# Kernel tuning notes

Hardware: AMD Instinct MI355X
Metric: run time of the kernel (lower is better)

The kernel has to match this reference:

```python
import jax, jax.numpy as jnp
import numpy as np

B = 65536

def setup_inputs() -> dict:
    key = jax.random.key(0)
    ks = jax.random.split(key, 8)
    x = jax.random.normal(ks[0], (B, 784), dtype=jnp.float32)
    conv_w = jnp.ones((3, 3), dtype=jnp.float32)  # Parameter(ones((3,3)))
    # Linear layers (stored as [in, out] so forward is x @ W + b)
    w1 = jax.random.normal(ks[1], (676, 100), dtype=jnp.float32) * 0.04
    b1 = jnp.zeros((100,), dtype=jnp.float32)
    w2 = jax.random.normal(ks[2], (100, 10), dtype=jnp.float32) * 0.1
    b2 = jnp.zeros((10,), dtype=jnp.float32)
    w3 = jax.random.normal(ks[3], (10, 10), dtype=jnp.float32) * 0.3
    b3 = jnp.zeros((10,), dtype=jnp.float32)
    return {"x": x, "conv_w": conv_w, "w1": w1, "b1": b1,
            "w2": w2, "b2": b2, "w3": w3, "b3": b3}


def _convolve_batch(x, conv_w):
    # x: [B, 28, 28]; valid 3x3 correlation (tensordot of patch with weight, no flip)
    lhs = x[:, None, :, :]                 # [B, 1, 28, 28] NCHW
    rhs = conv_w[None, None, :, :]         # [1, 1, 3, 3] OIHW
    out = jax.lax.conv_general_dilated(
        lhs, rhs, window_strides=(1, 1), padding="VALID",
        dimension_numbers=("NCHW", "OIHW", "NCHW"))
    return out[:, 0]                       # [B, 26, 26]


def reference(x, conv_w, w1, b1, w2, b2, w3, b3):
    b = x.shape[0]
    h = _convolve_batch(x.reshape(b, 28, 28), conv_w)   # [B, 26, 26]
    h = h.reshape(b, 676)
    h = jax.nn.relu(h @ w1 + b1)
    h = jax.nn.relu(h @ w2 + b2)
    return h @ w3 + b3                                   # [B, 10]
```

## Files before the change

kernel.cpp:

```cpp
#include <hip/hip_runtime.h>
#include <hip/hip_bf16.h>

#define K1 784
#define N1 100
#define KT 25
#define NTT 7
#define NTP 8

typedef __attribute__((ext_vector_type(8))) short bf16x8;
typedef __attribute__((ext_vector_type(4))) float f32x4;

__device__ __forceinline__ ushort f2bf(float f) {
    union { float f; unsigned u; } v; v.f = f;
    unsigned u = v.u;
    return (ushort)((u + 0x7FFFu + ((u >> 16) & 1u)) >> 16);
}

__device__ __forceinline__ bf16x8 pack_bf16x8(float4 a, float4 b) {
    union { unsigned u[4]; bf16x8 v; } r;
    asm("v_cvt_pk_bf16_f32 %0, %1, %2" : "=v"(r.u[0]) : "v"(a.x), "v"(a.y));
    asm("v_cvt_pk_bf16_f32 %0, %1, %2" : "=v"(r.u[1]) : "v"(a.z), "v"(a.w));
    asm("v_cvt_pk_bf16_f32 %0, %1, %2" : "=v"(r.u[2]) : "v"(b.x), "v"(b.y));
    asm("v_cvt_pk_bf16_f32 %0, %1, %2" : "=v"(r.u[3]) : "v"(b.z), "v"(b.w));
    return r.v;
}

__device__ __forceinline__ void gload_lds16(const void* g, void* l) {
    __builtin_amdgcn_global_load_lds(
        (const __attribute__((address_space(1))) void*)g,
        (__attribute__((address_space(3))) void*)l, 16, 0, 0);
}

__global__ void build_wp(const float* __restrict__ w1,
                         const float* __restrict__ conv_w,
                         ushort* __restrict__ wp) {
    int idx = blockIdx.x * blockDim.x + threadIdx.x;
    if (idx >= KT * NTP * 512) return;
    int j = idx & 7, lane = (idx >> 3) & 63, rest = idx >> 9;
    int nt = rest & 7, kt = rest >> 3;
    int k = kt * 32 + (lane >> 4) * 8 + j;
    int n = nt * 16 + (lane & 15);
    float w = 0.f;
    if (k < K1 && n < N1) {
        int py = k / 28, px = k % 28;
        #pragma unroll
        for (int dy = 0; dy < 3; ++dy) {
            int oy = py - dy; if (oy < 0 || oy > 25) continue;
            #pragma unroll
            for (int dx = 0; dx < 3; ++dx) {
                int ox = px - dx; if (ox < 0 || ox > 25) continue;
                w += conv_w[dy * 3 + dx] * w1[(oy * 26 + ox) * N1 + n];
            }
        }
    }
    wp[(size_t)(kt * NTP + nt) * 512 + lane * 8 + j] = f2bf(w);
}

__global__ __launch_bounds__(256, 2) void fused_mfma(
    const float* __restrict__ x, const ushort* __restrict__ wp,
    const float* __restrict__ b1, const float* __restrict__ w2,
    const float* __restrict__ b2, const float* __restrict__ w3,
    const float* __restrict__ b3, float* __restrict__ out)
{
    __shared__ __attribute__((aligned(16))) ushort bsm[3][NTP * 512];
    __shared__ float w2t[10][112];
    __shared__ float w3s[100];
    __shared__ float b1s[100];
    __shared__ float b2s[10], b3s[10];

    const int tid  = threadIdx.x;
    const int lane = tid & 63;
    const int lo16 = lane & 15, hi4 = lane >> 4;
    const int wid  = tid >> 6;
    const size_t rowbase = (size_t)blockIdx.x * 128 + wid * 32;

    for (int e = tid; e < 10 * 112; e += 256) w2t[e / 112][e % 112] = 0.f;
    __syncthreads();
    for (int e = tid; e < 1000; e += 256) w2t[e % 10][e / 10] = w2[e];
    for (int e = tid; e < 100; e += 256) { w3s[e] = w3[e]; b1s[e] = b1[e]; }
    if (tid < 10) { b2s[tid] = b2[tid]; b3s[tid] = b3[tid]; }
    __syncthreads();

    const float* xr0 = x + (rowbase + lo16) * K1;
    const float* xr1 = xr0 + (size_t)16 * K1;

    f32x4 acc[2][NTT];
    #pragma unroll
    for (int m = 0; m < 2; ++m)
        #pragma unroll
        for (int n = 0; n < NTT; ++n) { f32x4 z = {0.f,0.f,0.f,0.f}; acc[m][n] = z; }

    float4 xs[4][4];

#define STAGE(KTB)                                                            \
    { const ushort* src = wp + (size_t)(KTB) * (NTP * 512) + tid * 8;         \
      ushort* dst = &bsm[(KTB) % 3][tid * 8];                                 \
      gload_lds16(src, dst); gload_lds16(src + 2048, dst + 2048); }
#define LOADX(KTL, SLOT)                                                      \
    { int nb = (KTL) * 32 + hi4 * 8;                                          \
      if (nb > K1 - 8) nb = K1 - 8;               \
      xs[SLOT][0] = *reinterpret_cast<const float4*>(xr0 + nb);               \
      xs[SLOT][1] = *reinterpret_cast<const float4*>(xr0 + nb + 4);           \
      xs[SLOT][2] = *reinterpret_cast<const float4*>(xr1 + nb);               \
      xs[SLOT][3] = *reinterpret_cast<const float4*>(xr1 + nb + 4); }

    STAGE(0);
    __builtin_amdgcn_sched_barrier(0);
    LOADX(0, 0);
    __builtin_amdgcn_sched_barrier(0);
    STAGE(1);
    __builtin_amdgcn_sched_barrier(0);
    LOADX(1, 1);
    LOADX(2, 2);
    asm volatile("s_waitcnt vmcnt(14)" ::: "memory");
    __builtin_amdgcn_s_barrier();
    asm volatile("" ::: "memory");

    #pragma unroll
    for (int kt = 0; kt < KT; ++kt) {
        const int slot = kt % 4;
        const int bslot = kt % 3;
        if (kt <= KT - 3) {
            STAGE(kt + 2);
            __builtin_amdgcn_sched_barrier(0);
        }
        if (kt <= KT - 4) {
            LOADX(kt + 3, (kt + 3) % 4);
        }
        bf16x8 ah0 = pack_bf16x8(xs[slot][0], xs[slot][1]);
        bf16x8 ah1 = pack_bf16x8(xs[slot][2], xs[slot][3]);
        const ushort* bb = &bsm[bslot][lane * 8];
        #pragma unroll
        for (int nt = 0; nt < NTT; ++nt) {
            bf16x8 bh = *reinterpret_cast<const bf16x8*>(bb + nt * 512);
            acc[0][nt] = __builtin_amdgcn_mfma_f32_16x16x32_bf16(ah0, bh,
                                                          acc[0][nt], 0,0,0);
            acc[1][nt] = __builtin_amdgcn_mfma_f32_16x16x32_bf16(ah1, bh,
                                                          acc[1][nt], 0,0,0);
        }
        if (kt < KT - 1) {
            if (kt == 0)
                asm volatile("s_waitcnt vmcnt(14) lgkmcnt(0)" ::: "memory");
            else if (kt <= KT - 4)
                asm volatile("s_waitcnt vmcnt(10) lgkmcnt(0)" ::: "memory");
            else if (kt == KT - 3)
                asm volatile("s_waitcnt vmcnt(6) lgkmcnt(0)" ::: "memory");
            else
                asm volatile("s_waitcnt vmcnt(0) lgkmcnt(0)" ::: "memory");
            __builtin_amdgcn_s_barrier();
            asm volatile("" ::: "memory");
        }
    }
#undef STAGE
#undef LOADX

    __syncthreads();

    float h1v[2][NTT][4];
    #pragma unroll
    for (int m = 0; m < 2; ++m)
        #pragma unroll
        for (int nt = 0; nt < NTT; ++nt) {
            int col = nt * 16 + lo16;
            bool valid = col < N1;
            float bb = valid ? b1s[valid ? col : 0] : 0.f;
            #pragma unroll
            for (int r = 0; r < 4; ++r)
                h1v[m][nt][r] = valid ? fmaxf(acc[m][nt][r] + bb, 0.f) : 0.f;
        }

    const int jj = lo16;
    #pragma unroll
    for (int m = 0; m < 2; ++m) {
        float o[4] = {0.f, 0.f, 0.f, 0.f};
        #pragma unroll
        for (int j = 0; j < 10; ++j) {
            float pj[4] = {0.f, 0.f, 0.f, 0.f};
            #pragma unroll
            for (int nt = 0; nt < NTT; ++nt) {
                float wv = w2t[j][nt * 16 + lo16];
                #pragma unroll
                for (int r = 0; r < 4; ++r) pj[r] += h1v[m][nt][r] * wv;
            }
            #pragma unroll
            for (int mask = 8; mask >= 1; mask >>= 1)
                #pragma unroll
                for (int r = 0; r < 4; ++r)
                    pj[r] += __shfl_xor(pj[r], mask, 16);
            float w3v = (jj < 10) ? w3s[j * 10 + jj] : 0.f;
            #pragma unroll
            for (int r = 0; r < 4; ++r) {
                float h2 = fmaxf(pj[r] + b2s[j], 0.f);
                o[r] += h2 * w3v;
            }
        }
        if (jj < 10) {
            #pragma unroll
            for (int r = 0; r < 4; ++r)
                out[(rowbase + m * 16 + hi4 * 4 + r) * 10 + jj] = o[r] + b3s[jj];
        }
    }
}

extern "C" void kernel_launch(void* const* d_in, const int* in_sizes, int n_in,
                              void* d_out, int out_size, void* d_ws, size_t ws_size,
                              hipStream_t stream) {
    const float* x     = (const float*)d_in[0];
    const float* convw = (const float*)d_in[1];
    const float* w1    = (const float*)d_in[2];
    const float* b1    = (const float*)d_in[3];
    const float* w2    = (const float*)d_in[4];
    const float* b2    = (const float*)d_in[5];
    const float* w3    = (const float*)d_in[6];
    const float* b3    = (const float*)d_in[7];
    float* out  = (float*)d_out;
    ushort* wp  = (ushort*)d_ws;

    build_wp<<<(KT * NTP * 512 + 255) / 256, 256, 0, stream>>>(w1, convw, wp);
    fused_mfma<<<65536 / 128, 256, 0, stream>>>(x, wp, b1, w2, b2, w3, b3, out);
}
```

Measured before the change: 51.54 us.

## Restructure K-loop into double-buffered two-tile chunks with half the barriers

```diff
diff --git a/kernel.cpp b/kernel.cpp
--- a/kernel.cpp
+++ b/kernel.cpp
@@ -4,6 +4,7 @@
 #define K1 784
 #define N1 100
 #define KT 25
+#define NC 13
 #define NTT 7
 #define NTP 8
 
@@ -62,7 +63,7 @@
     const float* __restrict__ b2, const float* __restrict__ w3,
     const float* __restrict__ b3, float* __restrict__ out)
 {
-    __shared__ __attribute__((aligned(16))) ushort bsm[3][NTP * 512];
+    __shared__ __attribute__((aligned(16))) ushort bsm[2][2 * NTP * 512];
     __shared__ float w2t[10][112];
     __shared__ float w3s[100];
     __shared__ float b1s[100];
@@ -90,63 +91,61 @@
         #pragma unroll
         for (int n = 0; n < NTT; ++n) { f32x4 z = {0.f,0.f,0.f,0.f}; acc[m][n] = z; }
 
-    float4 xs[4][4];
-
-#define STAGE(KTB)                                                            \
-    { const ushort* src = wp + (size_t)(KTB) * (NTP * 512) + tid * 8;         \
-      ushort* dst = &bsm[(KTB) % 3][tid * 8];                                 \
-      gload_lds16(src, dst); gload_lds16(src + 2048, dst + 2048); }
-#define LOADX(KTL, SLOT)                                                      \
-    { int nb = (KTL) * 32 + hi4 * 8;                                          \
-      if (nb > K1 - 8) nb = K1 - 8;               \
-      xs[SLOT][0] = *reinterpret_cast<const float4*>(xr0 + nb);               \
-      xs[SLOT][1] = *reinterpret_cast<const float4*>(xr0 + nb + 4);           \
-      xs[SLOT][2] = *reinterpret_cast<const float4*>(xr1 + nb);               \
-      xs[SLOT][3] = *reinterpret_cast<const float4*>(xr1 + nb + 4); }
+    float4 xs[2][8];
+
+#define STAGE(C)                                                              \
+    { const ushort* src = wp + (size_t)(2 * (C)) * (NTP * 512) + tid * 8;     \
+      ushort* dst = &bsm[(C) % 2][tid * 8];                                   \
+      gload_lds16(src,        dst);                                           \
+      gload_lds16(src + 2048, dst + 2048);                                    \
+      gload_lds16(src + 4096, dst + 4096);                                    \
+      gload_lds16(src + 6144, dst + 6144); }
+#define LOADX(C)                                                              \
+    { int nb0 = (2 * (C)) * 32 + hi4 * 8;                                     \
+      int nb1 = nb0 + 32;                                                     \
+      if (nb0 > K1 - 8) nb0 = K1 - 8;                                         \
+      if (nb1 > K1 - 8) nb1 = K1 - 8;             \
+      xs[(C) % 2][0] = *reinterpret_cast<const float4*>(xr0 + nb0);           \
+      xs[(C) % 2][1] = *reinterpret_cast<const float4*>(xr0 + nb0 + 4);       \
+      xs[(C) % 2][2] = *reinterpret_cast<const float4*>(xr1 + nb0);           \
+      xs[(C) % 2][3] = *reinterpret_cast<const float4*>(xr1 + nb0 + 4);       \
+      xs[(C) % 2][4] = *reinterpret_cast<const float4*>(xr0 + nb1);           \
+      xs[(C) % 2][5] = *reinterpret_cast<const float4*>(xr0 + nb1 + 4);       \
+      xs[(C) % 2][6] = *reinterpret_cast<const float4*>(xr1 + nb1);           \
+      xs[(C) % 2][7] = *reinterpret_cast<const float4*>(xr1 + nb1 + 4); }
 
     STAGE(0);
     __builtin_amdgcn_sched_barrier(0);
-    LOADX(0, 0);
-    __builtin_amdgcn_sched_barrier(0);
-    STAGE(1);
-    __builtin_amdgcn_sched_barrier(0);
-    LOADX(1, 1);
-    LOADX(2, 2);
-    asm volatile("s_waitcnt vmcnt(14)" ::: "memory");
+    LOADX(0);
+    asm volatile("s_waitcnt vmcnt(8)" ::: "memory");
     __builtin_amdgcn_s_barrier();
     asm volatile("" ::: "memory");
 
     #pragma unroll
-    for (int kt = 0; kt < KT; ++kt) {
-        const int slot = kt % 4;
-        const int bslot = kt % 3;
-        if (kt <= KT - 3) {
-            STAGE(kt + 2);
+    for (int c = 0; c < NC; ++c) {
+        const int s = c % 2;
+        if (c < NC - 1) {
+            STAGE(c + 1);
             __builtin_amdgcn_sched_barrier(0);
-        }
-        if (kt <= KT - 4) {
-            LOADX(kt + 3, (kt + 3) % 4);
-        }
-        bf16x8 ah0 = pack_bf16x8(xs[slot][0], xs[slot][1]);
-        bf16x8 ah1 = pack_bf16x8(xs[slot][2], xs[slot][3]);
-        const ushort* bb = &bsm[bslot][lane * 8];
-        #pragma unroll
-        for (int nt = 0; nt < NTT; ++nt) {
-            bf16x8 bh = *reinterpret_cast<const bf16x8*>(bb + nt * 512);
-            acc[0][nt] = __builtin_amdgcn_mfma_f32_16x16x32_bf16(ah0, bh,
-                                                          acc[0][nt], 0,0,0);
-            acc[1][nt] = __builtin_amdgcn_mfma_f32_16x16x32_bf16(ah1, bh,
-                                                          acc[1][nt], 0,0,0);
-        }
-        if (kt < KT - 1) {
-            if (kt == 0)
-                asm volatile("s_waitcnt vmcnt(14) lgkmcnt(0)" ::: "memory");
-            else if (kt <= KT - 4)
-                asm volatile("s_waitcnt vmcnt(10) lgkmcnt(0)" ::: "memory");
-            else if (kt == KT - 3)
-                asm volatile("s_waitcnt vmcnt(6) lgkmcnt(0)" ::: "memory");
-            else
-                asm volatile("s_waitcnt vmcnt(0) lgkmcnt(0)" ::: "memory");
+            LOADX(c + 1);
+        }
+        #pragma unroll
+        for (int h = 0; h < 2; ++h) {
+            if (2 * c + h >= KT) break;
+            bf16x8 ah0 = pack_bf16x8(xs[s][h * 4 + 0], xs[s][h * 4 + 1]);
+            bf16x8 ah1 = pack_bf16x8(xs[s][h * 4 + 2], xs[s][h * 4 + 3]);
+            const ushort* bb = &bsm[s][h * (NTP * 512) + lane * 8];
+            #pragma unroll
+            for (int nt = 0; nt < NTT; ++nt) {
+                bf16x8 bh = *reinterpret_cast<const bf16x8*>(bb + nt * 512);
+                acc[0][nt] = __builtin_amdgcn_mfma_f32_16x16x32_bf16(ah0, bh,
+                                                              acc[0][nt], 0,0,0);
+                acc[1][nt] = __builtin_amdgcn_mfma_f32_16x16x32_bf16(ah1, bh,
+                                                              acc[1][nt], 0,0,0);
+            }
+        }
+        if (c < NC - 1) {
+            asm volatile("s_waitcnt vmcnt(8) lgkmcnt(0)" ::: "memory");
             __builtin_amdgcn_s_barrier();
             asm volatile("" ::: "memory");
         }
```

Result: slower. 53.50 us (+3.8%).
